# Optimization experiments

Measured on AMD Instinct MI355X. Metric: run time of the kernel, lower is better.

Reference implementation:

```python
import jax, jax.numpy as jnp
import numpy as np

N_NODES = 50000
N_EDGES = 800000
D_FEAT = 128
UNITS = 128


def setup_inputs() -> dict:
    key = jax.random.key(0)
    k1, k2, k3, k4 = jax.random.split(key, 4)
    x = jax.random.normal(k1, (N_NODES, D_FEAT), dtype=jnp.float32)
    source = jax.random.randint(k2, (N_EDGES,), 0, N_NODES, dtype=jnp.int32)
    target = jax.random.randint(k3, (N_EDGES,), 0, N_NODES, dtype=jnp.int32)
    W = jax.random.normal(k4, (D_FEAT, UNITS), dtype=jnp.float32) * (1.0 / np.sqrt(D_FEAT))
    b = jnp.zeros((UNITS,), dtype=jnp.float32)
    return {"x": x, "source": source, "target": target, "W": W, "b": b}


def _degree(idx, n_nodes):
    # in/out degree = segment-sum of unit edge weights; clamp to >= 1 (no self loops)
    deg = jnp.zeros((n_nodes,), dtype=jnp.float32).at[idx].add(1.0)
    return jnp.maximum(deg, 1.0)


def reference(x, source, target, W, b):
    n = x.shape[0]
    # degree_normalization == "in_out": sender scale from out-degree, receiver from in-degree
    sender_scale = jax.lax.rsqrt(_degree(source, n))[:, None]      # [N, 1]
    receiver_scale = jax.lax.rsqrt(_degree(target, n))[:, None]    # [N, 1]
    normalized = sender_scale * x                                  # [N, D]
    source_bcast = normalized[source]                              # [E, D] gather
    pooled = jax.ops.segment_sum(source_bcast, target, num_segments=n)  # [N, D] scatter-add
    pooled = receiver_scale * pooled
    # Dense(units, activation='relu', use_bias=True)
    return jax.nn.relu(pooled @ W + b)
```

## Files before the change

kernel.cpp:

```cpp
#include <hip/hip_runtime.h>
#include <hip/hip_bf16.h>

#define N_FEAT 128
#define EPT 8
#define CHUNK 2048
#define BSHIFT 8
#define MAXRANGE 256
#define CAP 8192
#define LSTR 66
#define ELCAP 512

typedef short bf16x8 __attribute__((ext_vector_type(8)));
typedef float f32x4  __attribute__((ext_vector_type(4)));

__device__ __forceinline__ unsigned short f2bf_rtne(float f) {
    unsigned u = __float_as_uint(f);
    u += 0x7fffu + ((u >> 16) & 1u);
    return (unsigned short)(u >> 16);
}
__device__ __forceinline__ float bf2f(unsigned short h) {
    return __uint_as_float((unsigned)h << 16);
}

__global__ __launch_bounds__(256) void scatter_kernel(const int* __restrict__ source,
                                                      const int* __restrict__ target,
                                                      int* __restrict__ curT,
                                                      int* __restrict__ curS,
                                                      unsigned int* __restrict__ pairsT,
                                                      unsigned char* __restrict__ srcB,
                                                      int E, int NB) {
    __shared__ unsigned int   lds_pairs[CHUNK];
    __shared__ unsigned short lds_sp[CHUNK];
    __shared__ int ct[MAXRANGE], cs[MAXRANGE];
    __shared__ int st[MAXRANGE], ss[MAXRANGE];
    __shared__ int gt[MAXRANGE], gs[MAXRANGE];
    int tid = threadIdx.x, b = blockIdx.x;
    int base = b * CHUNK;
    int cnt = E - base; if (cnt > CHUNK) cnt = CHUNK;

    int rs[EPT], rt[EPT];
    ct[tid] = 0; cs[tid] = 0;
    __syncthreads();
    #pragma unroll
    for (int j = 0; j < EPT; ++j) {
        int e = base + j * 256 + tid;
        if (e < E) {
            int s = source[e], t = target[e];
            rs[j] = s; rt[j] = t;
            atomicAdd(&ct[t >> BSHIFT], 1);
            atomicAdd(&cs[s >> BSHIFT], 1);
        }
    }
    __syncthreads();
    int vt = ct[tid], vs = cs[tid];
    st[tid] = vt; ss[tid] = vs;
    __syncthreads();
    #pragma unroll
    for (int off = 1; off < 256; off <<= 1) {
        int t1 = (tid >= off) ? st[tid - off] : 0;
        int t2 = (tid >= off) ? ss[tid - off] : 0;
        __syncthreads();
        st[tid] += t1; ss[tid] += t2;
        __syncthreads();
    }
    int et = st[tid] - vt, es = ss[tid] - vs;
    int gT = 0, gS = 0;
    if (tid < NB) {
        if (vt) gT = atomicAdd(&curT[tid], vt);
        if (vs) gS = atomicAdd(&curS[tid], vs);
    }
    __syncthreads();
    st[tid] = et; ss[tid] = es;
    ct[tid] = et; cs[tid] = es;
    gt[tid] = gT; gs[tid] = gS;
    __syncthreads();
    #pragma unroll
    for (int j = 0; j < EPT; ++j) {
        int e = base + j * 256 + tid;
        if (e < E) {
            int s = rs[j], t = rt[j];
            int k = t >> BSHIFT;
            int p = atomicAdd(&ct[k], 1);
            lds_pairs[p] = (unsigned)s | ((unsigned)t << 16);
            int k2 = s >> BSHIFT;
            int p2 = atomicAdd(&cs[k2], 1);
            lds_sp[p2] = (unsigned short)s;
        }
    }
    __syncthreads();
    for (int i = tid; i < cnt; i += 256) {
        unsigned w = lds_pairs[i];
        int k = w >> 24;
        pairsT[(size_t)k * CAP + gt[k] + (i - st[k])] = w;
        unsigned short sp = lds_sp[i];
        int k2 = sp >> 8;
        srcB[(size_t)k2 * CAP + gs[k2] + (i - ss[k2])] = (unsigned char)sp;
    }
}

__global__ __launch_bounds__(256) void prep_kernel(const unsigned char* __restrict__ srcB,
                                                   const unsigned int* __restrict__ pairsT,
                                                   const int* __restrict__ curT,
                                                   const int* __restrict__ curS,
                                                   const float* __restrict__ x,
                                                   const float* __restrict__ W,
                                                   unsigned short* __restrict__ xb,
                                                   int2* __restrict__ offs,
                                                   int* __restrict__ elist,
                                                   float* __restrict__ ri,
                                                   unsigned short* __restrict__ Whi,
                                                   unsigned short* __restrict__ Wlo,
                                                   int N, int NB) {
    __shared__ int hist[MAXRANGE];
    __shared__ int sb[MAXRANGE];
    __shared__ int excl[MAXRANGE];
    __shared__ int cur[MAXRANGE];
    __shared__ float so_l[MAXRANGE];
    int tid = threadIdx.x, b = blockIdx.x;

    if (b < NB) {
        hist[tid] = 0;
        __syncthreads();
        int cnt = curS[b];
        size_t base = (size_t)b * CAP;
        for (int i = tid; i < cnt; i += 256)
            atomicAdd(&hist[srcB[base + i]], 1);
        __syncthreads();
        {
            int d = hist[tid]; if (d < 1) d = 1;
            so_l[tid] = rsqrtf((float)d);
        }
        __syncthreads();
        int row0 = b << BSHIFT;
        int nrows = N - row0; if (nrows > 256) nrows = 256;
        if (nrows <= 0) return;
        int nf4 = nrows * (N_FEAT / 4);
        const float4* xr = (const float4*)(x + (size_t)row0 * N_FEAT);
        ushort4* xo = (ushort4*)(xb + (size_t)row0 * N_FEAT);
        for (int i = tid; i < nf4; i += 256) {
            float s = so_l[i >> 5];
            float4 v = xr[i];
            xo[i] = make_ushort4(f2bf_rtne(s * v.x), f2bf_rtne(s * v.y),
                                 f2bf_rtne(s * v.z), f2bf_rtne(s * v.w));
        }
    } else if (b < 2 * NB) {
        int bb = b - NB;
        hist[tid] = 0; cur[tid] = 0;
        __syncthreads();
        int cnt = curT[bb];
        int gbase = bb * CAP;
        for (int i = tid; i < cnt; i += 256)
            atomicAdd(&hist[(pairsT[(size_t)gbase + i] >> 16) & 255], 1);
        __syncthreads();
        int deg = hist[tid];
        sb[tid] = deg;
        __syncthreads();
        #pragma unroll
        for (int off = 1; off < 256; off <<= 1) {
            int t = (tid >= off) ? sb[tid - off] : 0;
            __syncthreads();
            sb[tid] += t;
            __syncthreads();
        }
        excl[tid] = sb[tid] - deg;
        __syncthreads();
        int node = (bb << BSHIFT) + tid;
        if (node < N) {
            int st0 = gbase + excl[tid];
            offs[node] = make_int2(st0, st0 + deg);
            int d = deg; if (d < 1) d = 1;
            ri[node] = rsqrtf((float)d);
        }
        for (int i = tid; i < cnt; i += 256) {
            unsigned w = pairsT[(size_t)gbase + i];
            int tl = (w >> 16) & 255;
            int pos = atomicAdd(&cur[tl], 1);
            elist[gbase + excl[tl] + pos] = (int)(w & 0xFFFFu);
        }
    } else {
        int idx = (b - 2 * NB) * 256 + tid;
        int lane = idx & 63;
        int ks = (idx >> 6) & 3;
        int ct2 = idx >> 8;
        int n  = ct2 * 16 + (lane & 15);
        int k0 = ks * 32 + (lane >> 4) * 8;
        unsigned short h[8], l[8];
        #pragma unroll
        for (int j = 0; j < 8; ++j) {
            float w = W[(k0 + j) * N_FEAT + n];
            unsigned short hh = f2bf_rtne(w);
            h[j] = hh;
            l[j] = f2bf_rtne(w - bf2f(hh));
        }
        size_t off = (size_t)idx * 8;
        *(ushort4*)(Whi + off)     = make_ushort4(h[0], h[1], h[2], h[3]);
        *(ushort4*)(Whi + off + 4) = make_ushort4(h[4], h[5], h[6], h[7]);
        *(ushort4*)(Wlo + off)     = make_ushort4(l[0], l[1], l[2], l[3]);
        *(ushort4*)(Wlo + off + 4) = make_ushort4(l[4], l[5], l[6], l[7]);
    }
}

__global__ __launch_bounds__(256) void agg_gemm_kernel(const unsigned short* __restrict__ xb,
                                                       const int* __restrict__ elist,
                                                       const int2* __restrict__ offs,
                                                       const float* __restrict__ ri,
                                                       const unsigned short* __restrict__ Whi,
                                                       const unsigned short* __restrict__ Wlo,
                                                       const float* __restrict__ bias,
                                                       float* __restrict__ out,
                                                       int N) {
    __shared__ unsigned int hi_l[16 * LSTR];
    __shared__ unsigned int lo_l[16 * LSTR];
    __shared__ int el[ELCAP];
    int tid  = threadIdx.x;
    int wave = tid >> 6, lane = tid & 63;
    int quad = lane >> 4, k16 = lane & 15;
    int rowbase = blockIdx.x * 16;
    const uint4* xr = (const uint4*)xb;

    int lastrow = rowbase + 15; if (lastrow > N - 1) lastrow = N - 1;
    int blk0 = offs[rowbase].x;
    int cnt  = offs[lastrow].y - blk0;
    int stg  = cnt < ELCAP ? cnt : ELCAP;
    for (int i = tid; i < stg; i += 256) el[i] = elist[blk0 + i];
    __syncthreads();

    int rl   = wave * 4 + quad;
    int node = rowbase + rl;
    int ls = 0, le = 0;
    float rr = 0.f;
    if (node < N) {
        int2 oe = offs[node];
        ls = oe.x - blk0; le = oe.y - blk0;
        rr = ri[node];
    }
    float acc[8] = {0.f, 0.f, 0.f, 0.f, 0.f, 0.f, 0.f, 0.f};
    for (int j = ls; j < le; j += 8) {
        uint4 u[8];
        #pragma unroll
        for (int t = 0; t < 8; ++t) {
            int idx = j + t;
            if (idx < le) {
                int e = (idx < stg) ? el[idx] : elist[blk0 + idx];
                u[t] = xr[(size_t)e * 16 + k16];
            }
        }
        #pragma unroll
        for (int t = 0; t < 8; ++t) {
            if (j + t < le) {
                acc[0] += __uint_as_float(u[t].x << 16);
                acc[1] += __uint_as_float(u[t].x & 0xffff0000u);
                acc[2] += __uint_as_float(u[t].y << 16);
                acc[3] += __uint_as_float(u[t].y & 0xffff0000u);
                acc[4] += __uint_as_float(u[t].z << 16);
                acc[5] += __uint_as_float(u[t].z & 0xffff0000u);
                acc[6] += __uint_as_float(u[t].w << 16);
                acc[7] += __uint_as_float(u[t].w & 0xffff0000u);
            }
        }
    }
    {
        unsigned int* hd = hi_l + rl * LSTR + 4 * k16;
        unsigned int* ld = lo_l + rl * LSTR + 4 * k16;
        #pragma unroll
        for (int d = 0; d < 4; ++d) {
            float v0 = acc[2 * d] * rr;
            float v1 = acc[2 * d + 1] * rr;
            unsigned short h0 = f2bf_rtne(v0), h1 = f2bf_rtne(v1);
            unsigned short l0 = f2bf_rtne(v0 - bf2f(h0));
            unsigned short l1 = f2bf_rtne(v1 - bf2f(h1));
            hd[d] = (unsigned)h0 | ((unsigned)h1 << 16);
            ld[d] = (unsigned)l0 | ((unsigned)l1 << 16);
        }
    }
    __syncthreads();

    bf16x8 Ahi[4], Alo[4];
    int m = k16;
    #pragma unroll
    for (int ks = 0; ks < 4; ++ks) {
        int a = m * LSTR + ks * 16 + quad * 4;
        Ahi[ks] = *(const bf16x8*)(hi_l + a);
        Alo[ks] = *(const bf16x8*)(lo_l + a);
    }
    const bf16x8* BH = (const bf16x8*)Whi;
    const bf16x8* BL = (const bf16x8*)Wlo;

    #pragma unroll
    for (int c = 0; c < 2; ++c) {
        int ct = wave * 2 + c;
        f32x4 acc2 = {0.f, 0.f, 0.f, 0.f};
        #pragma unroll
        for (int ks = 0; ks < 4; ++ks) {
            bf16x8 bh = BH[(ct * 4 + ks) * 64 + lane];
            bf16x8 bl = BL[(ct * 4 + ks) * 64 + lane];
            acc2 = __builtin_amdgcn_mfma_f32_16x16x32_bf16(Ahi[ks], bh, acc2, 0, 0, 0);
            acc2 = __builtin_amdgcn_mfma_f32_16x16x32_bf16(Alo[ks], bh, acc2, 0, 0, 0);
            acc2 = __builtin_amdgcn_mfma_f32_16x16x32_bf16(Ahi[ks], bl, acc2, 0, 0, 0);
        }
        int colc = ct * 16 + m;
        float bv = bias[colc];
        #pragma unroll
        for (int reg = 0; reg < 4; ++reg) {
            int r = rowbase + quad * 4 + reg;
            if (r < N)
                out[(size_t)r * N_FEAT + colc] = fmaxf(acc2[reg] + bv, 0.f);
        }
    }
}

extern "C" void kernel_launch(void* const* d_in, const int* in_sizes, int n_in,
                              void* d_out, int out_size, void* d_ws, size_t ws_size,
                              hipStream_t stream) {
    const float* x      = (const float*)d_in[0];
    const int*   source = (const int*)d_in[1];
    const int*   target = (const int*)d_in[2];
    const float* W      = (const float*)d_in[3];
    const float* bias   = (const float*)d_in[4];
    float*       out    = (float*)d_out;

    const int N = in_sizes[0] / N_FEAT;
    const int E = in_sizes[1];

    const int NB   = (N + MAXRANGE - 1) >> BSHIFT;
    const int NBLK = (E + CHUNK - 1) / CHUNK;

    uintptr_t p = (uintptr_t)d_ws;
    auto carve = [&](size_t bytes) {
        p = (p + 255) & ~(uintptr_t)255;
        uintptr_t r = p;
        p += bytes;
        return (void*)r;
    };
    int*            curs    = (int*)carve((size_t)2 * NB * sizeof(int));
    int*            curT    = curs;
    int*            curS    = curs + NB;
    unsigned int*   pairsT  = (unsigned int*)carve((size_t)NB * CAP * sizeof(unsigned int));
    int*            elist   = (int*)carve((size_t)NB * CAP * sizeof(int));
    unsigned char*  srcB    = (unsigned char*)carve((size_t)NB * CAP);
    float*          ri      = (float*)carve((size_t)N * sizeof(float));
    int2*           offs    = (int2*)carve((size_t)N * sizeof(int2));
    unsigned short* xb      = (unsigned short*)carve((size_t)N * N_FEAT * sizeof(unsigned short));
    unsigned short* Whi     = (unsigned short*)carve((size_t)N_FEAT * N_FEAT * sizeof(unsigned short));
    unsigned short* Wlo     = (unsigned short*)carve((size_t)N_FEAT * N_FEAT * sizeof(unsigned short));
    (void)ws_size; (void)n_in; (void)out_size;

    (void)hipMemsetAsync(curs, 0, (size_t)2 * NB * sizeof(int), stream);

    scatter_kernel<<<NBLK, 256, 0, stream>>>(source, target, curT, curS, pairsT, srcB, E, NB);
    prep_kernel<<<2 * NB + 8, 256, 0, stream>>>(srcB, pairsT, curT, curS, x, W,
                                                xb, offs, elist, ri, Whi, Wlo, N, NB);
    agg_gemm_kernel<<<(N + 15) / 16, 256, 0, stream>>>(xb, elist, offs, ri,
                                                       Whi, Wlo, bias, out, N);
}
```

Measured before the change: 157.0 us.

## Apply GEMM before aggregation so gather-sum runs on transformed features

Uses linearity to reorder the work: each node's scaled features are multiplied by W (split-bf16 MFMA) inside the prep kernel, producing a bf16 Y matrix. The aggregation kernel then gathers and sums rows of Y and applies the receiver scale, bias and ReLU, with no GEMM left in the per-node aggregation path. W splitting moves into extra blocks of the scatter kernel. Storing Y in bf16 after the GEMM changes where rounding happens, and the source-node blocks in prep now carry the GEMM work, which may unbalance that kernel.

```diff
diff --git a/kernel.cpp b/kernel.cpp
--- a/kernel.cpp
+++ b/kernel.cpp
@@ -8,7 +8,6 @@
 #define MAXRANGE 256
 #define CAP 8192
 #define LSTR 66
-#define ELCAP 512
 
 typedef short bf16x8 __attribute__((ext_vector_type(8)));
 typedef float f32x4  __attribute__((ext_vector_type(4)));
@@ -28,157 +27,19 @@
                                                       int* __restrict__ curS,
                                                       unsigned int* __restrict__ pairsT,
                                                       unsigned char* __restrict__ srcB,
-                                                      int E, int NB) {
+                                                      const float* __restrict__ W,
+                                                      unsigned short* __restrict__ Whi,
+                                                      unsigned short* __restrict__ Wlo,
+                                                      int E, int NB, int NBLK) {
     __shared__ unsigned int   lds_pairs[CHUNK];
     __shared__ unsigned short lds_sp[CHUNK];
     __shared__ int ct[MAXRANGE], cs[MAXRANGE];
     __shared__ int st[MAXRANGE], ss[MAXRANGE];
     __shared__ int gt[MAXRANGE], gs[MAXRANGE];
     int tid = threadIdx.x, b = blockIdx.x;
-    int base = b * CHUNK;
-    int cnt = E - base; if (cnt > CHUNK) cnt = CHUNK;
-
-    int rs[EPT], rt[EPT];
-    ct[tid] = 0; cs[tid] = 0;
-    __syncthreads();
-    #pragma unroll
-    for (int j = 0; j < EPT; ++j) {
-        int e = base + j * 256 + tid;
-        if (e < E) {
-            int s = source[e], t = target[e];
-            rs[j] = s; rt[j] = t;
-            atomicAdd(&ct[t >> BSHIFT], 1);
-            atomicAdd(&cs[s >> BSHIFT], 1);
-        }
-    }
-    __syncthreads();
-    int vt = ct[tid], vs = cs[tid];
-    st[tid] = vt; ss[tid] = vs;
-    __syncthreads();
-    #pragma unroll
-    for (int off = 1; off < 256; off <<= 1) {
-        int t1 = (tid >= off) ? st[tid - off] : 0;
-        int t2 = (tid >= off) ? ss[tid - off] : 0;
-        __syncthreads();
-        st[tid] += t1; ss[tid] += t2;
-        __syncthreads();
-    }
-    int et = st[tid] - vt, es = ss[tid] - vs;
-    int gT = 0, gS = 0;
-    if (tid < NB) {
-        if (vt) gT = atomicAdd(&curT[tid], vt);
-        if (vs) gS = atomicAdd(&curS[tid], vs);
-    }
-    __syncthreads();
-    st[tid] = et; ss[tid] = es;
-    ct[tid] = et; cs[tid] = es;
-    gt[tid] = gT; gs[tid] = gS;
-    __syncthreads();
-    #pragma unroll
-    for (int j = 0; j < EPT; ++j) {
-        int e = base + j * 256 + tid;
-        if (e < E) {
-            int s = rs[j], t = rt[j];
-            int k = t >> BSHIFT;
-            int p = atomicAdd(&ct[k], 1);
-            lds_pairs[p] = (unsigned)s | ((unsigned)t << 16);
-            int k2 = s >> BSHIFT;
-            int p2 = atomicAdd(&cs[k2], 1);
-            lds_sp[p2] = (unsigned short)s;
-        }
-    }
-    __syncthreads();
-    for (int i = tid; i < cnt; i += 256) {
-        unsigned w = lds_pairs[i];
-        int k = w >> 24;
-        pairsT[(size_t)k * CAP + gt[k] + (i - st[k])] = w;
-        unsigned short sp = lds_sp[i];
-        int k2 = sp >> 8;
-        srcB[(size_t)k2 * CAP + gs[k2] + (i - ss[k2])] = (unsigned char)sp;
-    }
-}
-
-__global__ __launch_bounds__(256) void prep_kernel(const unsigned char* __restrict__ srcB,
-                                                   const unsigned int* __restrict__ pairsT,
-                                                   const int* __restrict__ curT,
-                                                   const int* __restrict__ curS,
-                                                   const float* __restrict__ x,
-                                                   const float* __restrict__ W,
-                                                   unsigned short* __restrict__ xb,
-                                                   int2* __restrict__ offs,
-                                                   int* __restrict__ elist,
-                                                   float* __restrict__ ri,
-                                                   unsigned short* __restrict__ Whi,
-                                                   unsigned short* __restrict__ Wlo,
-                                                   int N, int NB) {
-    __shared__ int hist[MAXRANGE];
-    __shared__ int sb[MAXRANGE];
-    __shared__ int excl[MAXRANGE];
-    __shared__ int cur[MAXRANGE];
-    __shared__ float so_l[MAXRANGE];
-    int tid = threadIdx.x, b = blockIdx.x;
-
-    if (b < NB) {
-        hist[tid] = 0;
-        __syncthreads();
-        int cnt = curS[b];
-        size_t base = (size_t)b * CAP;
-        for (int i = tid; i < cnt; i += 256)
-            atomicAdd(&hist[srcB[base + i]], 1);
-        __syncthreads();
-        {
-            int d = hist[tid]; if (d < 1) d = 1;
-            so_l[tid] = rsqrtf((float)d);
-        }
-        __syncthreads();
-        int row0 = b << BSHIFT;
-        int nrows = N - row0; if (nrows > 256) nrows = 256;
-        if (nrows <= 0) return;
-        int nf4 = nrows * (N_FEAT / 4);
-        const float4* xr = (const float4*)(x + (size_t)row0 * N_FEAT);
-        ushort4* xo = (ushort4*)(xb + (size_t)row0 * N_FEAT);
-        for (int i = tid; i < nf4; i += 256) {
-            float s = so_l[i >> 5];
-            float4 v = xr[i];
-            xo[i] = make_ushort4(f2bf_rtne(s * v.x), f2bf_rtne(s * v.y),
-                                 f2bf_rtne(s * v.z), f2bf_rtne(s * v.w));
-        }
-    } else if (b < 2 * NB) {
-        int bb = b - NB;
-        hist[tid] = 0; cur[tid] = 0;
-        __syncthreads();
-        int cnt = curT[bb];
-        int gbase = bb * CAP;
-        for (int i = tid; i < cnt; i += 256)
-            atomicAdd(&hist[(pairsT[(size_t)gbase + i] >> 16) & 255], 1);
-        __syncthreads();
-        int deg = hist[tid];
-        sb[tid] = deg;
-        __syncthreads();
-        #pragma unroll
-        for (int off = 1; off < 256; off <<= 1) {
-            int t = (tid >= off) ? sb[tid - off] : 0;
-            __syncthreads();
-            sb[tid] += t;
-            __syncthreads();
-        }
-        excl[tid] = sb[tid] - deg;
-        __syncthreads();
-        int node = (bb << BSHIFT) + tid;
-        if (node < N) {
-            int st0 = gbase + excl[tid];
-            offs[node] = make_int2(st0, st0 + deg);
-            int d = deg; if (d < 1) d = 1;
-            ri[node] = rsqrtf((float)d);
-        }
-        for (int i = tid; i < cnt; i += 256) {
-            unsigned w = pairsT[(size_t)gbase + i];
-            int tl = (w >> 16) & 255;
-            int pos = atomicAdd(&cur[tl], 1);
-            elist[gbase + excl[tl] + pos] = (int)(w & 0xFFFFu);
-        }
-    } else {
-        int idx = (b - 2 * NB) * 256 + tid;
+
+    if (b >= NBLK) {
+        int idx = (b - NBLK) * 256 + tid;
         int lane = idx & 63;
         int ks = (idx >> 6) & 3;
         int ct2 = idx >> 8;
@@ -197,116 +58,257 @@
         *(ushort4*)(Whi + off + 4) = make_ushort4(h[4], h[5], h[6], h[7]);
         *(ushort4*)(Wlo + off)     = make_ushort4(l[0], l[1], l[2], l[3]);
         *(ushort4*)(Wlo + off + 4) = make_ushort4(l[4], l[5], l[6], l[7]);
-    }
-}
-
-__global__ __launch_bounds__(256) void agg_gemm_kernel(const unsigned short* __restrict__ xb,
-                                                       const int* __restrict__ elist,
-                                                       const int2* __restrict__ offs,
-                                                       const float* __restrict__ ri,
-                                                       const unsigned short* __restrict__ Whi,
-                                                       const unsigned short* __restrict__ Wlo,
-                                                       const float* __restrict__ bias,
-                                                       float* __restrict__ out,
-                                                       int N) {
-    __shared__ unsigned int hi_l[16 * LSTR];
-    __shared__ unsigned int lo_l[16 * LSTR];
-    __shared__ int el[ELCAP];
+        return;
+    }
+
+    int base = b * CHUNK;
+    int cnt = E - base; if (cnt > CHUNK) cnt = CHUNK;
+
+    int rs[EPT], rt[EPT];
+    ct[tid] = 0; cs[tid] = 0;
+    __syncthreads();
+    #pragma unroll
+    for (int j = 0; j < EPT; ++j) {
+        int e = base + j * 256 + tid;
+        if (e < E) {
+            int s = source[e], t = target[e];
+            rs[j] = s; rt[j] = t;
+            atomicAdd(&ct[t >> BSHIFT], 1);
+            atomicAdd(&cs[s >> BSHIFT], 1);
+        }
+    }
+    __syncthreads();
+    int vt = ct[tid], vs = cs[tid];
+    st[tid] = vt; ss[tid] = vs;
+    __syncthreads();
+    #pragma unroll
+    for (int off = 1; off < 256; off <<= 1) {
+        int t1 = (tid >= off) ? st[tid - off] : 0;
+        int t2 = (tid >= off) ? ss[tid - off] : 0;
+        __syncthreads();
+        st[tid] += t1; ss[tid] += t2;
+        __syncthreads();
+    }
+    int et = st[tid] - vt, es = ss[tid] - vs;
+    int gT = 0, gS = 0;
+    if (tid < NB) {
+        if (vt) gT = atomicAdd(&curT[tid], vt);
+        if (vs) gS = atomicAdd(&curS[tid], vs);
+    }
+    __syncthreads();
+    st[tid] = et; ss[tid] = es;
+    ct[tid] = et; cs[tid] = es;
+    gt[tid] = gT; gs[tid] = gS;
+    __syncthreads();
+    #pragma unroll
+    for (int j = 0; j < EPT; ++j) {
+        int e = base + j * 256 + tid;
+        if (e < E) {
+            int s = rs[j], t = rt[j];
+            int k = t >> BSHIFT;
+            int p = atomicAdd(&ct[k], 1);
+            lds_pairs[p] = (unsigned)s | ((unsigned)t << 16);
+            int k2 = s >> BSHIFT;
+            int p2 = atomicAdd(&cs[k2], 1);
+            lds_sp[p2] = (unsigned short)s;
+        }
+    }
+    __syncthreads();
+    for (int i = tid; i < cnt; i += 256) {
+        unsigned w = lds_pairs[i];
+        int k = w >> 24;
+        pairsT[(size_t)k * CAP + gt[k] + (i - st[k])] = w;
+        unsigned short sp = lds_sp[i];
+        int k2 = sp >> 8;
+        srcB[(size_t)k2 * CAP + gs[k2] + (i - ss[k2])] = (unsigned char)sp;
+    }
+}
+
+__global__ __launch_bounds__(256) void prep_kernel(const unsigned char* __restrict__ srcB,
+                                                   const unsigned int* __restrict__ pairsT,
+                                                   const int* __restrict__ curT,
+                                                   const int* __restrict__ curS,
+                                                   const float* __restrict__ x,
+                                                   const unsigned short* __restrict__ Whi,
+                                                   const unsigned short* __restrict__ Wlo,
+                                                   unsigned short* __restrict__ Y,
+                                                   int2* __restrict__ offs,
+                                                   int* __restrict__ elist,
+                                                   float* __restrict__ ri,
+                                                   int N, int NB) {
+    __shared__ int hist[MAXRANGE];
+    __shared__ int sb[MAXRANGE];
+    __shared__ int excl[MAXRANGE];
+    __shared__ int cur[MAXRANGE];
+    __shared__ float so_l[MAXRANGE];
+    __shared__ unsigned int hi_t[16 * LSTR];
+    __shared__ unsigned int lo_t[16 * LSTR];
+    int tid = threadIdx.x, b = blockIdx.x;
+    int wave = tid >> 6, lane = tid & 63;
+    int quad = lane >> 4, k16 = lane & 15;
+
+    if (b < NB) {
+        hist[tid] = 0;
+        __syncthreads();
+        int cnt = curS[b];
+        size_t base = (size_t)b * CAP;
+        for (int i = tid; i < cnt; i += 256)
+            atomicAdd(&hist[srcB[base + i]], 1);
+        __syncthreads();
+        {
+            int d = hist[tid]; if (d < 1) d = 1;
+            so_l[tid] = rsqrtf((float)d);
+        }
+        __syncthreads();
+        int row0 = b << BSHIFT;
+        int nrows = N - row0; if (nrows > 256) nrows = 256;
+        if (nrows <= 0) return;
+        const bf16x8* BH = (const bf16x8*)Whi;
+        const bf16x8* BL = (const bf16x8*)Wlo;
+        for (int t0 = 0; t0 < nrows; t0 += 16) {
+            for (int i = tid; i < 1024; i += 256) {
+                int r = i >> 6, dw = i & 63;
+                int gr = row0 + t0 + r;
+                float s = so_l[t0 + r];
+                float2 v = make_float2(0.f, 0.f);
+                if (gr < N) v = ((const float2*)x)[(size_t)gr * 64 + dw];
+                float v0 = s * v.x, v1 = s * v.y;
+                unsigned short h0 = f2bf_rtne(v0), h1 = f2bf_rtne(v1);
+                unsigned short l0 = f2bf_rtne(v0 - bf2f(h0));
+                unsigned short l1 = f2bf_rtne(v1 - bf2f(h1));
+                hi_t[r * LSTR + dw] = (unsigned)h0 | ((unsigned)h1 << 16);
+                lo_t[r * LSTR + dw] = (unsigned)l0 | ((unsigned)l1 << 16);
+            }
+            __syncthreads();
+            bf16x8 Ahi[4], Alo[4];
+            int m = k16;
+            #pragma unroll
+            for (int ks = 0; ks < 4; ++ks) {
+                int a = m * LSTR + ks * 16 + quad * 4;
+                Ahi[ks] = *(const bf16x8*)(hi_t + a);
+                Alo[ks] = *(const bf16x8*)(lo_t + a);
+            }
+            #pragma unroll
+            for (int c = 0; c < 2; ++c) {
+                int ctile = wave * 2 + c;
+                f32x4 acc = {0.f, 0.f, 0.f, 0.f};
+                #pragma unroll
+                for (int ks = 0; ks < 4; ++ks) {
+                    bf16x8 bh = BH[(ctile * 4 + ks) * 64 + lane];
+                    bf16x8 bl = BL[(ctile * 4 + ks) * 64 + lane];
+                    acc = __builtin_amdgcn_mfma_f32_16x16x32_bf16(Ahi[ks], bh, acc, 0, 0, 0);
+                    acc = __builtin_amdgcn_mfma_f32_16x16x32_bf16(Alo[ks], bh, acc, 0, 0, 0);
+                    acc = __builtin_amdgcn_mfma_f32_16x16x32_bf16(Ahi[ks], bl, acc, 0, 0, 0);
+                }
+                int colc = ctile * 16 + m;
+                #pragma unroll
+                for (int reg = 0; reg < 4; ++reg) {
+                    int gr = row0 + t0 + quad * 4 + reg;
+                    if (gr < N)
+                        Y[(size_t)gr * N_FEAT + colc] = f2bf_rtne(acc[reg]);
+                }
+            }
+            __syncthreads();
+        }
+    } else {
+        int bb = b - NB;
+        hist[tid] = 0; cur[tid] = 0;
+        __syncthreads();
+        int cnt = curT[bb];
+        int gbase = bb * CAP;
+        for (int i = tid; i < cnt; i += 256)
+            atomicAdd(&hist[(pairsT[(size_t)gbase + i] >> 16) & 255], 1);
+        __syncthreads();
+        int deg = hist[tid];
+        sb[tid] = deg;
+        __syncthreads();
+        #pragma unroll
+        for (int off = 1; off < 256; off <<= 1) {
+            int t = (tid >= off) ? sb[tid - off] : 0;
+            __syncthreads();
+            sb[tid] += t;
+            __syncthreads();
+        }
+        excl[tid] = sb[tid] - deg;
+        __syncthreads();
+        int node = (bb << BSHIFT) + tid;
+        if (node < N) {
+            int st0 = gbase + excl[tid];
+            offs[node] = make_int2(st0, st0 + deg);
+            int d = deg; if (d < 1) d = 1;
+            ri[node] = rsqrtf((float)d);
+        }
+        for (int i = tid; i < cnt; i += 256) {
+            unsigned w = pairsT[(size_t)gbase + i];
+            int tl = (w >> 16) & 255;
+            int pos = atomicAdd(&cur[tl], 1);
+            elist[gbase + excl[tl] + pos] = (int)(w & 0xFFFFu);
+        }
+    }
+}
+
+#define ACC8(u) { acc[0] += __uint_as_float((u).x << 16); \
+                  acc[1] += __uint_as_float((u).x & 0xffff0000u); \
+                  acc[2] += __uint_as_float((u).y << 16); \
+                  acc[3] += __uint_as_float((u).y & 0xffff0000u); \
+                  acc[4] += __uint_as_float((u).z << 16); \
+                  acc[5] += __uint_as_float((u).z & 0xffff0000u); \
+                  acc[6] += __uint_as_float((u).w << 16); \
+                  acc[7] += __uint_as_float((u).w & 0xffff0000u); }
+
+__global__ __launch_bounds__(128) void agg_kernel(const unsigned short* __restrict__ Y,
+                                                  const int* __restrict__ elist,
+                                                  const int2* __restrict__ offs,
+                                                  const float* __restrict__ ri,
+                                                  const float* __restrict__ bias,
+                                                  float* __restrict__ out,
+                                                  int N) {
     int tid  = threadIdx.x;
     int wave = tid >> 6, lane = tid & 63;
     int quad = lane >> 4, k16 = lane & 15;
-    int rowbase = blockIdx.x * 16;
-    const uint4* xr = (const uint4*)xb;
-
-    int lastrow = rowbase + 15; if (lastrow > N - 1) lastrow = N - 1;
-    int blk0 = offs[rowbase].x;
-    int cnt  = offs[lastrow].y - blk0;
-    int stg  = cnt < ELCAP ? cnt : ELCAP;
-    for (int i = tid; i < stg; i += 256) el[i] = elist[blk0 + i];
-    __syncthreads();
-
-    int rl   = wave * 4 + quad;
-    int node = rowbase + rl;
-    int ls = 0, le = 0;
-    float rr = 0.f;
-    if (node < N) {
-        int2 oe = offs[node];
-        ls = oe.x - blk0; le = oe.y - blk0;
-        rr = ri[node];
-    }
+    int node = blockIdx.x * 8 + wave * 4 + quad;
+    if (node >= N) return;
+    const uint4* yr = (const uint4*)Y;
+    int2 oe = offs[node];
+    float rr = ri[node];
     float acc[8] = {0.f, 0.f, 0.f, 0.f, 0.f, 0.f, 0.f, 0.f};
-    for (int j = ls; j < le; j += 8) {
-        uint4 u[8];
-        #pragma unroll
-        for (int t = 0; t < 8; ++t) {
-            int idx = j + t;
-            if (idx < le) {
-                int e = (idx < stg) ? el[idx] : elist[blk0 + idx];
-                u[t] = xr[(size_t)e * 16 + k16];
-            }
-        }
-        #pragma unroll
-        for (int t = 0; t < 8; ++t) {
-            if (j + t < le) {
-                acc[0] += __uint_as_float(u[t].x << 16);
-                acc[1] += __uint_as_float(u[t].x & 0xffff0000u);
-                acc[2] += __uint_as_float(u[t].y << 16);
-                acc[3] += __uint_as_float(u[t].y & 0xffff0000u);
-                acc[4] += __uint_as_float(u[t].z << 16);
-                acc[5] += __uint_as_float(u[t].z & 0xffff0000u);
-                acc[6] += __uint_as_float(u[t].w << 16);
-                acc[7] += __uint_as_float(u[t].w & 0xffff0000u);
-            }
-        }
-    }
-    {
-        unsigned int* hd = hi_l + rl * LSTR + 4 * k16;
-        unsigned int* ld = lo_l + rl * LSTR + 4 * k16;
-        #pragma unroll
-        for (int d = 0; d < 4; ++d) {
-            float v0 = acc[2 * d] * rr;
-            float v1 = acc[2 * d + 1] * rr;
-            unsigned short h0 = f2bf_rtne(v0), h1 = f2bf_rtne(v1);
-            unsigned short l0 = f2bf_rtne(v0 - bf2f(h0));
-            unsigned short l1 = f2bf_rtne(v1 - bf2f(h1));
-            hd[d] = (unsigned)h0 | ((unsigned)h1 << 16);
-            ld[d] = (unsigned)l0 | ((unsigned)l1 << 16);
-        }
-    }
-    __syncthreads();
-
-    bf16x8 Ahi[4], Alo[4];
-    int m = k16;
-    #pragma unroll
-    for (int ks = 0; ks < 4; ++ks) {
-        int a = m * LSTR + ks * 16 + quad * 4;
-        Ahi[ks] = *(const bf16x8*)(hi_l + a);
-        Alo[ks] = *(const bf16x8*)(lo_l + a);
-    }
-    const bf16x8* BH = (const bf16x8*)Whi;
-    const bf16x8* BL = (const bf16x8*)Wlo;
-
-    #pragma unroll
-    for (int c = 0; c < 2; ++c) {
-        int ct = wave * 2 + c;
-        f32x4 acc2 = {0.f, 0.f, 0.f, 0.f};
-        #pragma unroll
-        for (int ks = 0; ks < 4; ++ks) {
-            bf16x8 bh = BH[(ct * 4 + ks) * 64 + lane];
-            bf16x8 bl = BL[(ct * 4 + ks) * 64 + lane];
-            acc2 = __builtin_amdgcn_mfma_f32_16x16x32_bf16(Ahi[ks], bh, acc2, 0, 0, 0);
-            acc2 = __builtin_amdgcn_mfma_f32_16x16x32_bf16(Alo[ks], bh, acc2, 0, 0, 0);
-            acc2 = __builtin_amdgcn_mfma_f32_16x16x32_bf16(Ahi[ks], bl, acc2, 0, 0, 0);
-        }
-        int colc = ct * 16 + m;
-        float bv = bias[colc];
-        #pragma unroll
-        for (int reg = 0; reg < 4; ++reg) {
-            int r = rowbase + quad * 4 + reg;
-            if (r < N)
-                out[(size_t)r * N_FEAT + colc] = fmaxf(acc2[reg] + bv, 0.f);
-        }
-    }
+    int j = oe.x, je = oe.y;
+    for (; j + 8 <= je; j += 8) {
+        int e0 = elist[j],     e1 = elist[j + 1];
+        int e2 = elist[j + 2], e3 = elist[j + 3];
+        int e4 = elist[j + 4], e5 = elist[j + 5];
+        int e6 = elist[j + 6], e7 = elist[j + 7];
+        uint4 u0 = yr[(size_t)e0 * 16 + k16];
+        uint4 u1 = yr[(size_t)e1 * 16 + k16];
+        uint4 u2 = yr[(size_t)e2 * 16 + k16];
+        uint4 u3 = yr[(size_t)e3 * 16 + k16];
+        uint4 u4 = yr[(size_t)e4 * 16 + k16];
+        uint4 u5 = yr[(size_t)e5 * 16 + k16];
+        uint4 u6 = yr[(size_t)e6 * 16 + k16];
+        uint4 u7 = yr[(size_t)e7 * 16 + k16];
+        ACC8(u0) ACC8(u1) ACC8(u2) ACC8(u3)
+        ACC8(u4) ACC8(u5) ACC8(u6) ACC8(u7)
+    }
+    for (; j < je; ++j) {
+        int e = elist[j];
+        uint4 u = yr[(size_t)e * 16 + k16];
+        ACC8(u)
+    }
+    int f0 = k16 * 8;
+    const float4* bp = (const float4*)(bias + f0);
+    float4 b0 = bp[0], b1 = bp[1];
+    float4 o0, o1;
+    o0.x = fmaxf(acc[0] * rr + b0.x, 0.f);
+    o0.y = fmaxf(acc[1] * rr + b0.y, 0.f);
+    o0.z = fmaxf(acc[2] * rr + b0.z, 0.f);
+    o0.w = fmaxf(acc[3] * rr + b0.w, 0.f);
+    o1.x = fmaxf(acc[4] * rr + b1.x, 0.f);
+    o1.y = fmaxf(acc[5] * rr + b1.y, 0.f);
+    o1.z = fmaxf(acc[6] * rr + b1.z, 0.f);
+    o1.w = fmaxf(acc[7] * rr + b1.w, 0.f);
+    float4* op = (float4*)(out + (size_t)node * N_FEAT + f0);
+    op[0] = o0;
+    op[1] = o1;
 }
 
 extern "C" void kernel_launch(void* const* d_in, const int* in_sizes, int n_in,
@@ -340,16 +342,16 @@
     unsigned char*  srcB    = (unsigned char*)carve((size_t)NB * CAP);
     float*          ri      = (float*)carve((size_t)N * sizeof(float));
     int2*           offs    = (int2*)carve((size_t)N * sizeof(int2));
-    unsigned short* xb      = (unsigned short*)carve((size_t)N * N_FEAT * sizeof(unsigned short));
+    unsigned short* Y       = (unsigned short*)carve((size_t)N * N_FEAT * sizeof(unsigned short));
     unsigned short* Whi     = (unsigned short*)carve((size_t)N_FEAT * N_FEAT * sizeof(unsigned short));
     unsigned short* Wlo     = (unsigned short*)carve((size_t)N_FEAT * N_FEAT * sizeof(unsigned short));
     (void)ws_size; (void)n_in; (void)out_size;
 
     (void)hipMemsetAsync(curs, 0, (size_t)2 * NB * sizeof(int), stream);
 
-    scatter_kernel<<<NBLK, 256, 0, stream>>>(source, target, curT, curS, pairsT, srcB, E, NB);
-    prep_kernel<<<2 * NB + 8, 256, 0, stream>>>(srcB, pairsT, curT, curS, x, W,
-                                                xb, offs, elist, ri, Whi, Wlo, N, NB);
-    agg_gemm_kernel<<<(N + 15) / 16, 256, 0, stream>>>(xb, elist, offs, ri,
-                                                       Whi, Wlo, bias, out, N);
-}
+    scatter_kernel<<<NBLK + 8, 256, 0, stream>>>(source, target, curT, curS, pairsT, srcB,
+                                                 W, Whi, Wlo, E, NB, NBLK);
+    prep_kernel<<<2 * NB, 256, 0, stream>>>(srcB, pairsT, curT, curS, x, Whi, Wlo,
+                                            Y, offs, elist, ri, N, NB);
+    agg_kernel<<<(N + 7) / 8, 128, 0, stream>>>(Y, elist, offs, ri, bias, out, N);
+}
```

Result: slower. 174.5 us (+11.1%).
